# Optimization experiments

Measured on AMD Instinct MI355X. Metric: run time of the kernel, lower is better.

Reference implementation:

```python
import jax, jax.numpy as jnp
import numpy as np

B, L, D_MODEL = 2, 1024, 1024
D_STATE, D_CONV, EXPAND = 16, 4, 2
D_INNER = D_MODEL * EXPAND
LN_EPS = 1e-5


def setup_inputs() -> dict:
    key = jax.random.key(0)
    ks = jax.random.split(key, 6)
    g = lambda k, shape, scale: (jax.random.normal(k, shape, jnp.float32) * scale)
    x = jax.random.normal(ks[0], (B, L, D_MODEL), jnp.float32)
    in_proj_w = g(ks[1], (2 * D_INNER, D_MODEL), D_MODEL ** -0.5)
    conv_w = g(ks[2], (D_INNER, D_CONV), D_CONV ** -0.5)   # depthwise kernel
    conv_b = jnp.zeros((D_INNER,), jnp.float32)
    x_proj_w = g(ks[3], (2 * D_STATE + 1, D_INNER), D_INNER ** -0.5)
    A_log = jnp.tile(jnp.log(jnp.arange(1, D_STATE + 1, dtype=jnp.float32)), (D_INNER, 1))
    D_param = jnp.ones((D_INNER,), jnp.float32)
    dt_w = g(ks[4], (D_INNER, 1), 1.0)
    dt_b = jnp.full((D_INNER,), -4.0, jnp.float32)
    out_w = g(ks[5], (D_MODEL, D_INNER), D_INNER ** -0.5)
    ln_g = jnp.ones((D_INNER,), jnp.float32)
    ln_b = jnp.zeros((D_INNER,), jnp.float32)
    return dict(x=x, in_proj_w=in_proj_w, conv_w=conv_w, conv_b=conv_b,
                x_proj_w=x_proj_w, A_log=A_log, D_param=D_param,
                dt_w=dt_w, dt_b=dt_b, out_w=out_w, ln_g=ln_g, ln_b=ln_b)


def _forward(x, in_proj_w, conv_w, conv_b, x_proj_w, A_log, D_param,
             dt_w, dt_b, out_w, ln_g, ln_b):
    Lq = x.shape[1]
    xz = jnp.einsum('bld,ed->ble', x, in_proj_w)            # (B,L,2*Di)
    xb, z = xz[..., :D_INNER], xz[..., D_INNER:]
    # causal depthwise conv1d (pad left d_conv-1, valid conv == torch pad+truncate)
    xpad = jnp.pad(xb, ((0, 0), (D_CONV - 1, 0), (0, 0)))
    xc = conv_b
    for k in range(D_CONV):
        xc = xc + xpad[:, k:k + Lq, :] * conv_w[:, k]
    xb = jax.nn.silu(xc)
    proj = jnp.einsum('bld,ed->ble', xb, x_proj_w)          # (B,L,2N+1)
    dt_in = proj[..., :1]
    Bp = proj[..., 1:1 + D_STATE]                            # (B,L,N)
    Cp = proj[..., 1 + D_STATE:]                             # (B,L,N)
    dt = jax.nn.softplus(dt_in * dt_w[:, 0] + dt_b)          # (B,L,Di)
    A = -jnp.exp(A_log)                                      # (Di,N)
    dA = jnp.exp(dt[..., None] * A)                          # (B,L,Di,N)
    x_scaled = (xb * dt)[..., None] * Bp[..., None, :]       # (B,L,Di,N)
    # linear recurrence h[t] = dA[t]*h[t-1] + x_scaled[t] via associative scan
    def comb(a, b):
        return (a[0] * b[0], b[0] * a[1] + b[1])
    _, h = jax.lax.associative_scan(comb, (dA, x_scaled), axis=1)
    y = jnp.einsum('bldn,bln->bld', h, Cp) + xb * D_param    # (B,L,Di)
    mu = jnp.mean(y, axis=-1, keepdims=True)
    var = jnp.var(y, axis=-1, keepdims=True)
    y = (y - mu) / jnp.sqrt(var + LN_EPS) * ln_g + ln_b
    y = y * jax.nn.silu(z)
    return jnp.einsum('bld,ed->ble', y, out_w)               # (B,L,d_model)


def reference(x, in_proj_w, conv_w, conv_b, x_proj_w, A_log, D_param,
              dt_w, dt_b, out_w, ln_g, ln_b):
    return _forward(x, in_proj_w, conv_w, conv_b, x_proj_w, A_log, D_param,
                    dt_w, dt_b, out_w, ln_g, ln_b)
```

## Files before the change

kernel.cpp:

```cpp
#include <hip/hip_runtime.h>

typedef unsigned short u16;
typedef unsigned int u32;
typedef __bf16 bf16x8 __attribute__((ext_vector_type(8)));
typedef float f32x4 __attribute__((ext_vector_type(4)));
typedef unsigned short ushort8 __attribute__((ext_vector_type(8)));

__device__ __forceinline__ float bf2f(u16 b) {
    return __uint_as_float(((u32)b) << 16);
}
__device__ __forceinline__ u16 f2bf(float f) {
    u32 u = __float_as_uint(f);
    return (u16)((u + 0x7fffu + ((u >> 16) & 1u)) >> 16);
}

#define P_CONVW 0
#define P_CONVB 8192
#define P_ALOG  10240
#define P_DPAR  43008
#define P_DTW   45056
#define P_DTB   47104
#define P_LNG   49152
#define P_LNB   51200
#define P_TOTAL 53248

#define CCH 32
#define CT  32
#define CHUNKTOT 2097152
#define PSTRIDE 128

#define CV_X   524288
#define CV_W1  1572864
#define CV_TOT 2097152

struct ParamPtrs { const void* p[8]; };

__global__ __launch_bounds__(256) void canon_all(ParamPtrs pp, float* __restrict__ cpar,
                                                 const void* __restrict__ sx,
                                                 const void* __restrict__ sw1,
                                                 const void* __restrict__ swo,
                                                 u16* __restrict__ cx,
                                                 const void* __restrict__ sxp,
                                                 u16* __restrict__ wpad,
                                                 const u16* __restrict__ dp) {
    const bool isbf = (dp[0] != 0);
    const int blk = blockIdx.x;
    const int tid = threadIdx.x;
    if (blk < 8192) {
        const int i = blk * 256 + tid;
        const void* src;
        int off;
        if (i < CV_X)       { src = sx;  off = i; }
        else if (i < CV_W1) { src = sw1; off = i - CV_X; }
        else                { src = swo; off = i - CV_W1; }
        if (isbf) {
            ((uint2*)cx)[i] = ((const uint2*)src)[off];
        } else {
            const float4 v = ((const float4*)src)[off];
            uint2 o;
            o.x = (u32)f2bf(v.x) | ((u32)f2bf(v.y) << 16);
            o.y = (u32)f2bf(v.z) | ((u32)f2bf(v.w) << 16);
            ((uint2*)cx)[i] = o;
        }
    } else if (blk < 8400) {
        const int i = (blk - 8192) * 256 + tid;
        int seg, off;
        if (i < P_CONVB)      { seg = 0; off = i; }
        else if (i < P_ALOG)  { seg = 1; off = i - P_CONVB; }
        else if (i < P_DPAR)  { seg = 2; off = i - P_ALOG; }
        else if (i < P_DTW)   { seg = 3; off = i - P_DPAR; }
        else if (i < P_DTB)   { seg = 4; off = i - P_DTW; }
        else if (i < P_LNG)   { seg = 5; off = i - P_DTB; }
        else if (i < P_LNB)   { seg = 6; off = i - P_LNG; }
        else                  { seg = 7; off = i - P_LNB; }
        cpar[i] = isbf ? bf2f(((const u16*)pp.p[seg])[off]) : ((const float*)pp.p[seg])[off];
    } else {
        const int i = (blk - 8400) * 256 + tid;
        const int idx = i * 4;
        const int row = idx >> 11;
        u16 o[4];
#pragma unroll
        for (int q = 0; q < 4; ++q) {
            float v = 0.f;
            if (row < 33)
                v = isbf ? bf2f(((const u16*)sxp)[idx + q]) : ((const float*)sxp)[idx + q];
            o[q] = f2bf(v);
        }
        *(uint2*)&wpad[idx] = *(uint2*)o;
    }
}

__device__ __forceinline__ bf16x8 lds_frag(const char* smem, u32 base, int row, int kk,
                                           int quad, u32 xorv) {
    const u32 addr = (base + (u32)(row * 128 + kk * 64 + quad * 16)) ^ xorv;
    return *(const bf16x8*)(smem + addr);
}

template <int MODE>
__global__ __launch_bounds__(512, 2) void gemm8(const u16* __restrict__ A,
                                                const u16* __restrict__ Bw,
                                                void* __restrict__ C,
                                                int M, int N, int Kseg,
                                                int lda, int ldb) {
    extern __shared__ char smem[];
    const int bm = blockIdx.x, bn = blockIdx.y;
    const int kbase = blockIdx.z * Kseg;
    const int tid = threadIdx.x;
    const int lane = tid & 63, wave = tid >> 6;
    const int wm = wave >> 2, wn = wave & 3;
    const int l16 = lane & 15, quad = lane >> 4;
    const int NT = Kseg >> 6;
    const u32 xorv = (u32)((l16 & 7) << 4);

    const int rIss = wave * 8 + (lane >> 3);
    const int logC = (lane & 7) ^ ((lane >> 3) & 7);
    size_t aSrc[2], bSrc[4];
#pragma unroll
    for (int j = 0; j < 2; ++j)
        aSrc[j] = (size_t)(bm * 128 + j * 64 + rIss) * lda + logC * 8 + kbase;
#pragma unroll
    for (int j = 0; j < 4; ++j)
        bSrc[j] = (size_t)(bn * 256 + j * 64 + rIss) * ldb + logC * 8 + kbase;
    const u32 ldsW = (u32)(wave * 1024);

#define SG_A(slot, j, kel) __builtin_amdgcn_global_load_lds( \
        (const u32*)(A + aSrc[j] + (kel)), (u32*)(smem + (slot) + (j) * 8192 + ldsW), 16, 0, 0)
#define SG_B(slot, j, kel) __builtin_amdgcn_global_load_lds( \
        (const u32*)(Bw + bSrc[j] + (kel)), (u32*)(smem + (slot) + (j) * 8192 + ldsW), 16, 0, 0)

    const u32 sA0 = 0, sA1 = 16384, sA2 = 32768;
    const u32 sB0 = 49152, sB1 = 81920, sB2 = 114688;

    SG_A(sA0, 0, 0); SG_A(sA0, 1, 0);
    SG_B(sB0, 0, 0); SG_B(sB0, 1, 0); SG_B(sB0, 2, 0); SG_B(sB0, 3, 0);
    SG_A(sA1, 0, 64); SG_A(sA1, 1, 64);
    SG_B(sB1, 0, 64); SG_B(sB1, 1, 64); SG_B(sB1, 2, 64); SG_B(sB1, 3, 64);
    asm volatile("s_waitcnt vmcnt(6)" ::: "memory");
    __builtin_amdgcn_s_barrier();
    __builtin_amdgcn_sched_barrier(0);

    u32 curA = sA0, nxtA = sA1, stgA = sA2;
    u32 curB = sB0, nxtB = sB1, stgB = sB2;
    int kStage = 128;

    f32x4 acc[4][4] = {};
    bf16x8 a[4][2], b[4][2];

    for (int t = 0; t < NT; ++t) {
        const bool doStage = (t + 2) < NT;
#pragma unroll
        for (int mt = 0; mt < 4; ++mt)
#pragma unroll
            for (int kk = 0; kk < 2; ++kk)
                a[mt][kk] = lds_frag(smem, curA, wm * 64 + mt * 16 + l16, kk, quad, xorv);
#pragma unroll
        for (int nt = 0; nt < 2; ++nt)
#pragma unroll
            for (int kk = 0; kk < 2; ++kk)
                b[nt][kk] = lds_frag(smem, curB, wn * 64 + nt * 16 + l16, kk, quad, xorv);
        if (doStage) { SG_A(stgA, 0, kStage); SG_A(stgA, 1, kStage); SG_B(stgB, 0, kStage); }
        __builtin_amdgcn_s_setprio(1);
#pragma unroll
        for (int mt = 0; mt < 4; ++mt)
#pragma unroll
            for (int nt = 0; nt < 2; ++nt)
#pragma unroll
                for (int kk = 0; kk < 2; ++kk)
                    acc[mt][nt] = __builtin_amdgcn_mfma_f32_16x16x32_bf16(
                        a[mt][kk], b[nt][kk], acc[mt][nt], 0, 0, 0);
        __builtin_amdgcn_s_setprio(0);
#pragma unroll
        for (int nt = 2; nt < 4; ++nt)
#pragma unroll
            for (int kk = 0; kk < 2; ++kk)
                b[nt][kk] = lds_frag(smem, curB, wn * 64 + nt * 16 + l16, kk, quad, xorv);
        if (doStage) { SG_B(stgB, 1, kStage); SG_B(stgB, 2, kStage); SG_B(stgB, 3, kStage); }
        __builtin_amdgcn_s_setprio(1);
#pragma unroll
        for (int mt = 0; mt < 4; ++mt)
#pragma unroll
            for (int nt = 2; nt < 4; ++nt)
#pragma unroll
                for (int kk = 0; kk < 2; ++kk)
                    acc[mt][nt] = __builtin_amdgcn_mfma_f32_16x16x32_bf16(
                        a[mt][kk], b[nt][kk], acc[mt][nt], 0, 0, 0);
        __builtin_amdgcn_s_setprio(0);
        if (t < NT - 1) {
            if (doStage) asm volatile("s_waitcnt vmcnt(6)" ::: "memory");
            else         asm volatile("s_waitcnt vmcnt(0)" ::: "memory");
            __builtin_amdgcn_s_barrier();
            __builtin_amdgcn_sched_barrier(0);
            u32 tA = curA; curA = nxtA; nxtA = stgA; stgA = tA;
            u32 tB = curB; curB = nxtB; nxtB = stgB; stgB = tB;
            kStage += 64;
        }
    }
#undef SG_A
#undef SG_B

    float* Cf = (float*)C + (MODE == 1 ? (size_t)blockIdx.z * M * N : (size_t)0);
#pragma unroll
    for (int mt = 0; mt < 4; ++mt) {
#pragma unroll
        for (int r = 0; r < 4; ++r) {
            const int row = bm * 128 + wm * 64 + mt * 16 + quad * 4 + r;
#pragma unroll
            for (int nt = 0; nt < 4; ++nt) {
                const int col = bn * 256 + wn * 64 + nt * 16 + l16;
                if (MODE == 0)
                    ((u16*)C)[(size_t)row * N + col] = f2bf(acc[mt][nt][r]);
                else
                    Cf[(size_t)row * N + col] = acc[mt][nt][r];
            }
        }
    }
}

template <int MODE>
__global__ __launch_bounds__(256) void gemm_bt(const u16* __restrict__ A,
                                               const u16* __restrict__ Bw,
                                               void* __restrict__ C,
                                               int M, int N, int Kseg,
                                               int lda, int ldb) {
    const int bm = blockIdx.x;
    const int bn = blockIdx.y;
    const int kbase = blockIdx.z * Kseg;
    const int tid = threadIdx.x;
    const int lane = tid & 63;
    const int wave = tid >> 6;
    const int wm = wave >> 1, wn = wave & 1;
    const int l16 = lane & 15, quad = lane >> 4;

    __shared__ __align__(16) u16 sA[128 * 32];
    __shared__ __align__(16) u16 sB[128 * 32];

    f32x4 acc[4][4] = {};

    const int rsub = lane >> 2;
    const int csub = (lane & 3) * 8;

    for (int k0 = 0; k0 < Kseg; k0 += 32) {
        const int kc = kbase + k0 + csub;
        __syncthreads();
#pragma unroll
        for (int q = 0; q < 2; ++q) {
            const int g = wave + 4 * q;
            const int row = g * 16 + rsub;
            __builtin_amdgcn_global_load_lds(
                (const u32*)&A[(size_t)(bm * 128 + row) * lda + kc],
                (u32*)&sA[g * 512], 16, 0, 0);
            __builtin_amdgcn_global_load_lds(
                (const u32*)&Bw[(size_t)(bn * 128 + row) * ldb + kc],
                (u32*)&sB[g * 512], 16, 0, 0);
        }
        __syncthreads();

        bf16x8 af[4], bg[4];
#pragma unroll
        for (int t = 0; t < 4; ++t) {
            af[t] = *(const bf16x8*)&sA[(wm * 64 + t * 16 + l16) * 32 + quad * 8];
            bg[t] = *(const bf16x8*)&sB[(wn * 64 + t * 16 + l16) * 32 + quad * 8];
        }
#pragma unroll
        for (int mt = 0; mt < 4; ++mt)
#pragma unroll
            for (int nt = 0; nt < 4; ++nt)
                acc[mt][nt] = __builtin_amdgcn_mfma_f32_16x16x32_bf16(
                    af[mt], bg[nt], acc[mt][nt], 0, 0, 0);
    }

    float* Cf = (float*)C + (MODE == 1 ? (size_t)blockIdx.z * M * N : (size_t)0);
#pragma unroll
    for (int mt = 0; mt < 4; ++mt) {
#pragma unroll
        for (int r = 0; r < 4; ++r) {
            const int row = bm * 128 + wm * 64 + mt * 16 + quad * 4 + r;
#pragma unroll
            for (int nt = 0; nt < 4; ++nt) {
                const int col = bn * 128 + wn * 64 + nt * 16 + l16;
                if (MODE == 0)
                    ((u16*)C)[(size_t)row * N + col] = f2bf(acc[mt][nt][r]);
                else
                    Cf[(size_t)row * N + col] = acc[mt][nt][r];
            }
        }
    }
}

__global__ __launch_bounds__(256) void reduce_parts(const float* __restrict__ src,
                                                    float* __restrict__ dst,
                                                    int n4, int parts) {
    const int i = blockIdx.x * 256 + threadIdx.x;
    if (i >= n4) return;
    float4 s = ((const float4*)src)[i];
    for (int p = 1; p < parts; ++p) {
        const float4 v = ((const float4*)src)[(size_t)p * n4 + i];
        s.x += v.x; s.y += v.y; s.z += v.z; s.w += v.w;
    }
    ((float4*)dst)[i] = s;
}

__global__ __launch_bounds__(256) void conv_silu(const u16* __restrict__ xz,
                                                 const float* __restrict__ par,
                                                 u16* __restrict__ xb16) {
    const int idx = blockIdx.x * 256 + threadIdx.x;
    const int d8 = idx & 255;
    const int bl = idx >> 8;
    const int l = bl & 1023;
    const int d0 = d8 * 8;

    float acc[8];
    {
        const float4 b0 = *(const float4*)&par[P_CONVB + d0];
        const float4 b1 = *(const float4*)&par[P_CONVB + d0 + 4];
        acc[0] = b0.x; acc[1] = b0.y; acc[2] = b0.z; acc[3] = b0.w;
        acc[4] = b1.x; acc[5] = b1.y; acc[6] = b1.z; acc[7] = b1.w;
    }
    float warr[8][4];
#pragma unroll
    for (int q = 0; q < 8; ++q) {
        const float4 w = *(const float4*)&par[P_CONVW + (d0 + q) * 4];
        warr[q][0] = w.x; warr[q][1] = w.y; warr[q][2] = w.z; warr[q][3] = w.w;
    }
#pragma unroll
    for (int k = 0; k < 4; ++k) {
        const int ls = l + k - 3;
        if (ls >= 0) {
            const ushort8 xv = *(const ushort8*)&xz[(size_t)(bl + k - 3) * 4096 + d0];
#pragma unroll
            for (int q = 0; q < 8; ++q)
                acc[q] = fmaf(bf2f(xv[q]), warr[q][k], acc[q]);
        }
    }
    u16 o[8];
#pragma unroll
    for (int q = 0; q < 8; ++q) {
        const float s = acc[q] / (1.f + __expf(-acc[q]));
        o[q] = f2bf(s);
    }
    *(uint4*)&xb16[(size_t)bl * 2048 + d0] = *(uint4*)o;
}

__global__ __launch_bounds__(256) void scan_p1(const u16* __restrict__ xb16,
                                               const float* __restrict__ proj,
                                               const float* __restrict__ par,
                                               float* __restrict__ PS) {
    const int tid = threadIdx.x;
    const int half = tid & 1;
    const int d = blockIdx.x * 128 + (tid >> 1);
    const int c = blockIdx.y;
    const int b = blockIdx.z;
    const int nb = half * 8;
    __shared__ float sp[CT][33];
    const size_t row0 = (size_t)b * 1024 + c * CT;
    for (int f = tid; f < CT * 33; f += 256) {
        const int i = f / 33, j = f - i * 33;
        sp[i][j] = proj[(row0 + i) * PSTRIDE + j];
    }
    float Aneg[8];
#pragma unroll
    for (int n = 0; n < 8; ++n) Aneg[n] = -__expf(par[P_ALOG + d * 16 + nb + n]);
    const float dtw = par[P_DTW + d], dtb = par[P_DTB + d];
    __syncthreads();

    float h[8] = {}, P[8];
#pragma unroll
    for (int n = 0; n < 8; ++n) P[n] = 1.f;

    float xv = bf2f(xb16[row0 * 2048 + d]);
    for (int i = 0; i < CT; ++i) {
        const float xv_next = (i + 1 < CT) ? bf2f(xb16[(row0 + i + 1) * 2048 + d]) : 0.f;
        const float darg = fmaf(sp[i][0], dtw, dtb);
        const float dt = (darg > 20.f) ? darg : __logf(1.f + __expf(darg));
        const float xdt = xv * dt;
#pragma unroll
        for (int n = 0; n < 8; ++n) {
            const float dA = __expf(dt * Aneg[n]);
            P[n] *= dA;
            h[n] = fmaf(dA, h[n], xdt * sp[i][1 + nb + n]);
        }
        xv = xv_next;
    }
    const size_t base = (((size_t)b * CCH + c) * 16) * 2048 + d;
#pragma unroll
    for (int n = 0; n < 8; ++n) {
        PS[base + (size_t)(nb + n) * 2048] = P[n];
        PS[CHUNKTOT + base + (size_t)(nb + n) * 2048] = h[n];
    }
}

__global__ __launch_bounds__(256) void scan_comb(const float* __restrict__ PS,
                                                 float* __restrict__ H) {
    const int t = blockIdx.x * 256 + threadIdx.x;
    const int d = t & 2047;
    const int n = (t >> 11) & 15;
    const int b = t >> 15;
    float h = 0.f;
#pragma unroll
    for (int c = 0; c < CCH; ++c) {
        const size_t idx = (((size_t)b * CCH + c) * 16 + n) * 2048 + d;
        H[idx] = h;
        h = fmaf(PS[idx], h, PS[CHUNKTOT + idx]);
    }
}

__global__ __launch_bounds__(256) void scan_p2(const u16* __restrict__ xb16,
                                               const float* __restrict__ proj,
                                               const float* __restrict__ par,
                                               const float* __restrict__ H,
                                               u16* __restrict__ y) {
    const int tid = threadIdx.x;
    const int half = tid & 1;
    const int d = blockIdx.x * 128 + (tid >> 1);
    const int c = blockIdx.y;
    const int b = blockIdx.z;
    const int nb = half * 8;
    __shared__ float sp[CT][33];
    const size_t row0 = (size_t)b * 1024 + c * CT;
    for (int f = tid; f < CT * 33; f += 256) {
        const int i = f / 33, j = f - i * 33;
        sp[i][j] = proj[(row0 + i) * PSTRIDE + j];
    }
    float Aneg[8], h[8];
    const size_t hbase = (((size_t)b * CCH + c) * 16) * 2048 + d;
#pragma unroll
    for (int n = 0; n < 8; ++n) {
        Aneg[n] = -__expf(par[P_ALOG + d * 16 + nb + n]);
        h[n] = H[hbase + (size_t)(nb + n) * 2048];
    }
    const float dtw = par[P_DTW + d], dtb = par[P_DTB + d];
    const float Dp = par[P_DPAR + d];
    __syncthreads();

    float xv = bf2f(xb16[row0 * 2048 + d]);
    for (int i = 0; i < CT; ++i) {
        const float xv_next = (i + 1 < CT) ? bf2f(xb16[(row0 + i + 1) * 2048 + d]) : 0.f;
        const float darg = fmaf(sp[i][0], dtw, dtb);
        const float dt = (darg > 20.f) ? darg : __logf(1.f + __expf(darg));
        const float xdt = xv * dt;
        float acc = 0.f;
#pragma unroll
        for (int n = 0; n < 8; ++n) {
            const float dA = __expf(dt * Aneg[n]);
            h[n] = fmaf(dA, h[n], xdt * sp[i][1 + nb + n]);
            acc = fmaf(h[n], sp[i][17 + nb + n], acc);
        }
        acc += __shfl_xor(acc, 1);
        if (!half)
            y[(row0 + i) * 2048 + d] = f2bf(fmaf(xv, Dp, acc));
        xv = xv_next;
    }
}

__global__ __launch_bounds__(256) void ln_silu(const u16* __restrict__ y,
                                               const u16* __restrict__ xz,
                                               const float* __restrict__ par,
                                               u16* __restrict__ yn) {
    const int row = blockIdx.x;
    const int tid = threadIdx.x;
    const int lane = tid & 63, wave = tid >> 6;
    const int d0 = tid * 8;
    const ushort8 vy = *(const ushort8*)&y[(size_t)row * 2048 + d0];
    float v[8];
    float s = 0.f, s2 = 0.f;
#pragma unroll
    for (int i = 0; i < 8; ++i) {
        v[i] = bf2f(vy[i]);
        s += v[i];
        s2 = fmaf(v[i], v[i], s2);
    }
    s += __shfl_xor(s, 1); s2 += __shfl_xor(s2, 1);
    s += __shfl_xor(s, 2); s2 += __shfl_xor(s2, 2);
    s += __shfl_xor(s, 4); s2 += __shfl_xor(s2, 4);
    s += __shfl_xor(s, 8); s2 += __shfl_xor(s2, 8);
    s += __shfl_xor(s, 16); s2 += __shfl_xor(s2, 16);
    s += __shfl_xor(s, 32); s2 += __shfl_xor(s2, 32);
    __shared__ float rs[4], rs2[4];
    if (lane == 0) { rs[wave] = s; rs2[wave] = s2; }
    __syncthreads();
    const float ts = rs[0] + rs[1] + rs[2] + rs[3];
    const float ts2 = rs2[0] + rs2[1] + rs2[2] + rs2[3];
    const float mu = ts * (1.f / 2048.f);
    const float var = ts2 * (1.f / 2048.f) - mu * mu;
    const float rstd = rsqrtf(var + 1e-5f);

    const ushort8 vz = *(const ushort8*)&xz[(size_t)row * 4096 + 2048 + d0];
    float g[8], bb[8];
    {
        const float4 g0 = *(const float4*)&par[P_LNG + d0];
        const float4 g1 = *(const float4*)&par[P_LNG + d0 + 4];
        g[0] = g0.x; g[1] = g0.y; g[2] = g0.z; g[3] = g0.w;
        g[4] = g1.x; g[5] = g1.y; g[6] = g1.z; g[7] = g1.w;
        const float4 b0 = *(const float4*)&par[P_LNB + d0];
        const float4 b1 = *(const float4*)&par[P_LNB + d0 + 4];
        bb[0] = b0.x; bb[1] = b0.y; bb[2] = b0.z; bb[3] = b0.w;
        bb[4] = b1.x; bb[5] = b1.y; bb[6] = b1.z; bb[7] = b1.w;
    }
    u16 o[8];
#pragma unroll
    for (int i = 0; i < 8; ++i) {
        float t = (v[i] - mu) * rstd * g[i] + bb[i];
        const float z = bf2f(vz[i]);
        t *= z / (1.f + __expf(-z));
        o[i] = f2bf(t);
    }
    *(uint4*)&yn[(size_t)row * 2048 + d0] = *(uint4*)o;
}

extern "C" void kernel_launch(void* const* d_in, const int* in_sizes, int n_in,
                              void* d_out, int out_size, void* d_ws, size_t ws_size,
                              hipStream_t stream) {
    const void* x         = d_in[0];
    const void* in_proj_w = d_in[1];
    const void* conv_w    = d_in[2];
    const void* conv_b    = d_in[3];
    const void* x_proj_w  = d_in[4];
    const void* A_log     = d_in[5];
    const void* D_param   = d_in[6];
    const void* dt_w      = d_in[7];
    const void* dt_b      = d_in[8];
    const void* out_w     = d_in[9];
    const void* ln_g      = d_in[10];
    const void* ln_b      = d_in[11];
    const u16* dp = (const u16*)D_param;

    float* cpar = (float*)d_ws;
    u16* cx     = (u16*)(cpar + P_TOTAL);
    u16* cw1    = cx + 2097152;
    u16* cwo    = cw1 + 4194304;
    u16* xz     = cwo + 2097152;
    u16* xb16   = xz + 8388608;
    u16* y      = xb16 + 4194304;
    u16* wpad   = y + 4194304;
    float* proj = (float*)(wpad + 262144);
    float* PS   = proj + 262144;
    float* H    = PS + 2 * CHUNKTOT;
    float* gpart = H + CHUNKTOT;
    float* xpart = gpart;
    u16* yn      = xb16;

    static bool attrSet = false;
    if (!attrSet) {
        hipFuncSetAttribute(reinterpret_cast<const void*>(&gemm8<0>),
                            hipFuncAttributeMaxDynamicSharedMemorySize, 147456);
        hipFuncSetAttribute(reinterpret_cast<const void*>(&gemm8<1>),
                            hipFuncAttributeMaxDynamicSharedMemorySize, 147456);
        attrSet = true;
    }

    ParamPtrs pp;
    pp.p[0] = conv_w; pp.p[1] = conv_b; pp.p[2] = A_log; pp.p[3] = D_param;
    pp.p[4] = dt_w;   pp.p[5] = dt_b;   pp.p[6] = ln_g;  pp.p[7] = ln_b;
    canon_all<<<8656, 256, 0, stream>>>(pp, cpar, x, in_proj_w, out_w, cx,
                                        x_proj_w, wpad, dp);

    gemm8<0><<<dim3(16, 16, 1), 512, 147456, stream>>>(cx, cw1, xz,
                                                       2048, 4096, 1024, 1024, 1024);
    conv_silu<<<2048, 256, 0, stream>>>(xz, cpar, xb16);
    gemm_bt<1><<<dim3(16, 1, 16), 256, 0, stream>>>(xb16, wpad, xpart, 2048, 128, 128, 2048, 2048);
    reduce_parts<<<256, 256, 0, stream>>>(xpart, proj, 65536, 16);
    scan_p1<<<dim3(16, CCH, 2), 256, 0, stream>>>(xb16, proj, cpar, PS);
    scan_comb<<<256, 256, 0, stream>>>(PS, H);
    scan_p2<<<dim3(16, CCH, 2), 256, 0, stream>>>(xb16, proj, cpar, H, y);
    ln_silu<<<2048, 256, 0, stream>>>(y, xz, cpar, yn);
    gemm8<1><<<dim3(16, 4, 4), 512, 147456, stream>>>(yn, cwo, gpart,
                                                      2048, 1024, 512, 2048, 2048);
    reduce_parts<<<2048, 256, 0, stream>>>(gpart, (float*)d_out, 524288, 4);
}
```

Measured before the change: 234.3 us.

## Fuse chunked scan passes into one kernel with in-block chunk combine

Replaces the three-kernel chunked scan (partial pass, global combine, second pass) with a single kernel. Each block handles 4 channels across all chunks, combines the chunk carries in shared memory, and reads proj directly from global memory instead of staging it in LDS. This removes the PS/H global round trips and two launches, at the cost of fewer, differently shaped blocks and uncoalesced strided xb16 reads. It also halves the split-K factor of the output GEMM, giving fewer partial sums to reduce.

```diff
diff --git a/kernel.cpp b/kernel.cpp
--- a/kernel.cpp
+++ b/kernel.cpp
@@ -341,114 +341,106 @@
     *(uint4*)&xb16[(size_t)bl * 2048 + d0] = *(uint4*)o;
 }
 
-__global__ __launch_bounds__(256) void scan_p1(const u16* __restrict__ xb16,
-                                               const float* __restrict__ proj,
-                                               const float* __restrict__ par,
-                                               float* __restrict__ PS) {
+__global__ __launch_bounds__(256) void scan_fused(const u16* __restrict__ xb16,
+                                                  const float* __restrict__ proj,
+                                                  const float* __restrict__ par,
+                                                  u16* __restrict__ y) {
     const int tid = threadIdx.x;
-    const int half = tid & 1;
-    const int d = blockIdx.x * 128 + (tid >> 1);
-    const int c = blockIdx.y;
+    const int h2 = tid & 1;
+    const int dsub = (tid >> 1) & 3;
+    const int c = tid >> 3;
+    const int d = blockIdx.x * 4 + dsub;
     const int b = blockIdx.z;
-    const int nb = half * 8;
-    __shared__ float sp[CT][33];
-    const size_t row0 = (size_t)b * 1024 + c * CT;
-    for (int f = tid; f < CT * 33; f += 256) {
-        const int i = f / 33, j = f - i * 33;
-        sp[i][j] = proj[(row0 + i) * PSTRIDE + j];
-    }
+    const int nb = h2 * 8;
+
+    __shared__ float Pl[CCH][4][17];
+    __shared__ float Sl[CCH][4][17];
+
     float Aneg[8];
 #pragma unroll
     for (int n = 0; n < 8; ++n) Aneg[n] = -__expf(par[P_ALOG + d * 16 + nb + n]);
     const float dtw = par[P_DTW + d], dtb = par[P_DTB + d];
+    const float Dp = par[P_DPAR + d];
+
+    const size_t row0 = (size_t)b * 1024 + (size_t)c * CT;
+
+    {
+        float hl[8] = {}, P[8];
+#pragma unroll
+        for (int n = 0; n < 8; ++n) P[n] = 1.f;
+        float xv = bf2f(xb16[row0 * 2048 + d]);
+        for (int i = 0; i < CT; ++i) {
+            const float xv_next = (i + 1 < CT) ? bf2f(xb16[(row0 + i + 1) * 2048 + d]) : 0.f;
+            const size_t pb = (row0 + i) * PSTRIDE;
+            const float dtin = proj[pb];
+            const float4 q0 = *(const float4*)&proj[pb + nb + 0];
+            const float4 q1 = *(const float4*)&proj[pb + nb + 4];
+            const float4 q2 = *(const float4*)&proj[pb + nb + 8];
+            const float Bv[8] = {q0.y, q0.z, q0.w, q1.x, q1.y, q1.z, q1.w, q2.x};
+            const float darg = fmaf(dtin, dtw, dtb);
+            const float dt = (darg > 20.f) ? darg : __logf(1.f + __expf(darg));
+            const float xdt = xv * dt;
+#pragma unroll
+            for (int n = 0; n < 8; ++n) {
+                const float dA = __expf(dt * Aneg[n]);
+                P[n] *= dA;
+                hl[n] = fmaf(dA, hl[n], xdt * Bv[n]);
+            }
+            xv = xv_next;
+        }
+#pragma unroll
+        for (int n = 0; n < 8; ++n) {
+            Pl[c][dsub][nb + n] = P[n];
+            Sl[c][dsub][nb + n] = hl[n];
+        }
+    }
     __syncthreads();
 
-    float h[8] = {}, P[8];
-#pragma unroll
-    for (int n = 0; n < 8; ++n) P[n] = 1.f;
-
-    float xv = bf2f(xb16[row0 * 2048 + d]);
-    for (int i = 0; i < CT; ++i) {
-        const float xv_next = (i + 1 < CT) ? bf2f(xb16[(row0 + i + 1) * 2048 + d]) : 0.f;
-        const float darg = fmaf(sp[i][0], dtw, dtb);
-        const float dt = (darg > 20.f) ? darg : __logf(1.f + __expf(darg));
-        const float xdt = xv * dt;
-#pragma unroll
-        for (int n = 0; n < 8; ++n) {
-            const float dA = __expf(dt * Aneg[n]);
-            P[n] *= dA;
-            h[n] = fmaf(dA, h[n], xdt * sp[i][1 + nb + n]);
-        }
-        xv = xv_next;
-    }
-    const size_t base = (((size_t)b * CCH + c) * 16) * 2048 + d;
-#pragma unroll
-    for (int n = 0; n < 8; ++n) {
-        PS[base + (size_t)(nb + n) * 2048] = P[n];
-        PS[CHUNKTOT + base + (size_t)(nb + n) * 2048] = h[n];
-    }
-}
-
-__global__ __launch_bounds__(256) void scan_comb(const float* __restrict__ PS,
-                                                 float* __restrict__ H) {
-    const int t = blockIdx.x * 256 + threadIdx.x;
-    const int d = t & 2047;
-    const int n = (t >> 11) & 15;
-    const int b = t >> 15;
-    float h = 0.f;
-#pragma unroll
-    for (int c = 0; c < CCH; ++c) {
-        const size_t idx = (((size_t)b * CCH + c) * 16 + n) * 2048 + d;
-        H[idx] = h;
-        h = fmaf(PS[idx], h, PS[CHUNKTOT + idx]);
-    }
-}
-
-__global__ __launch_bounds__(256) void scan_p2(const u16* __restrict__ xb16,
-                                               const float* __restrict__ proj,
-                                               const float* __restrict__ par,
-                                               const float* __restrict__ H,
-                                               u16* __restrict__ y) {
-    const int tid = threadIdx.x;
-    const int half = tid & 1;
-    const int d = blockIdx.x * 128 + (tid >> 1);
-    const int c = blockIdx.y;
-    const int b = blockIdx.z;
-    const int nb = half * 8;
-    __shared__ float sp[CT][33];
-    const size_t row0 = (size_t)b * 1024 + c * CT;
-    for (int f = tid; f < CT * 33; f += 256) {
-        const int i = f / 33, j = f - i * 33;
-        sp[i][j] = proj[(row0 + i) * PSTRIDE + j];
-    }
-    float Aneg[8], h[8];
-    const size_t hbase = (((size_t)b * CCH + c) * 16) * 2048 + d;
-#pragma unroll
-    for (int n = 0; n < 8; ++n) {
-        Aneg[n] = -__expf(par[P_ALOG + d * 16 + nb + n]);
-        h[n] = H[hbase + (size_t)(nb + n) * 2048];
-    }
-    const float dtw = par[P_DTW + d], dtb = par[P_DTB + d];
-    const float Dp = par[P_DPAR + d];
+    if (tid < 64) {
+        const int dd = tid >> 4, n = tid & 15;
+        float hh = 0.f;
+#pragma unroll
+        for (int cc = 0; cc < CCH; ++cc) {
+            const float p = Pl[cc][dd][n];
+            const float s = Sl[cc][dd][n];
+            Pl[cc][dd][n] = hh;
+            hh = fmaf(p, hh, s);
+        }
+    }
     __syncthreads();
 
-    float xv = bf2f(xb16[row0 * 2048 + d]);
-    for (int i = 0; i < CT; ++i) {
-        const float xv_next = (i + 1 < CT) ? bf2f(xb16[(row0 + i + 1) * 2048 + d]) : 0.f;
-        const float darg = fmaf(sp[i][0], dtw, dtb);
-        const float dt = (darg > 20.f) ? darg : __logf(1.f + __expf(darg));
-        const float xdt = xv * dt;
-        float acc = 0.f;
-#pragma unroll
-        for (int n = 0; n < 8; ++n) {
-            const float dA = __expf(dt * Aneg[n]);
-            h[n] = fmaf(dA, h[n], xdt * sp[i][1 + nb + n]);
-            acc = fmaf(h[n], sp[i][17 + nb + n], acc);
-        }
-        acc += __shfl_xor(acc, 1);
-        if (!half)
-            y[(row0 + i) * 2048 + d] = f2bf(fmaf(xv, Dp, acc));
-        xv = xv_next;
+    {
+        float hl[8];
+#pragma unroll
+        for (int n = 0; n < 8; ++n) hl[n] = Pl[c][dsub][nb + n];
+        float xv = bf2f(xb16[row0 * 2048 + d]);
+        for (int i = 0; i < CT; ++i) {
+            const float xv_next = (i + 1 < CT) ? bf2f(xb16[(row0 + i + 1) * 2048 + d]) : 0.f;
+            const size_t pb = (row0 + i) * PSTRIDE;
+            const float dtin = proj[pb];
+            const float4 q0 = *(const float4*)&proj[pb + nb + 0];
+            const float4 q1 = *(const float4*)&proj[pb + nb + 4];
+            const float4 q2 = *(const float4*)&proj[pb + nb + 8];
+            const float4 r0 = *(const float4*)&proj[pb + 16 + nb + 0];
+            const float4 r1 = *(const float4*)&proj[pb + 16 + nb + 4];
+            const float4 r2 = *(const float4*)&proj[pb + 16 + nb + 8];
+            const float Bv[8] = {q0.y, q0.z, q0.w, q1.x, q1.y, q1.z, q1.w, q2.x};
+            const float Cv[8] = {r0.y, r0.z, r0.w, r1.x, r1.y, r1.z, r1.w, r2.x};
+            const float darg = fmaf(dtin, dtw, dtb);
+            const float dt = (darg > 20.f) ? darg : __logf(1.f + __expf(darg));
+            const float xdt = xv * dt;
+            float acc = 0.f;
+#pragma unroll
+            for (int n = 0; n < 8; ++n) {
+                const float dA = __expf(dt * Aneg[n]);
+                hl[n] = fmaf(dA, hl[n], xdt * Bv[n]);
+                acc = fmaf(hl[n], Cv[n], acc);
+            }
+            acc += __shfl_xor(acc, 1);
+            if (!h2)
+                y[(row0 + i) * 2048 + d] = f2bf(fmaf(xv, Dp, acc));
+            xv = xv_next;
+        }
     }
 }
 
@@ -559,11 +551,9 @@
     conv_silu<<<2048, 256, 0, stream>>>(xz, cpar, xb16);
     gemm_bt<1><<<dim3(16, 1, 16), 256, 0, stream>>>(xb16, wpad, xpart, 2048, 128, 128, 2048, 2048);
     reduce_parts<<<256, 256, 0, stream>>>(xpart, proj, 65536, 16);
-    scan_p1<<<dim3(16, CCH, 2), 256, 0, stream>>>(xb16, proj, cpar, PS);
-    scan_comb<<<256, 256, 0, stream>>>(PS, H);
-    scan_p2<<<dim3(16, CCH, 2), 256, 0, stream>>>(xb16, proj, cpar, H, y);
+    scan_fused<<<dim3(512, 1, 2), 256, 0, stream>>>(xb16, proj, cpar, y);
     ln_silu<<<2048, 256, 0, stream>>>(y, xz, cpar, yn);
-    gemm8<1><<<dim3(16, 4, 4), 512, 147456, stream>>>(yn, cwo, gpart,
-                                                      2048, 1024, 512, 2048, 2048);
-    reduce_parts<<<2048, 256, 0, stream>>>(gpart, (float*)d_out, 524288, 4);
-}
+    gemm8<1><<<dim3(16, 4, 2), 512, 147456, stream>>>(yn, cwo, gpart,
+                                                      2048, 1024, 1024, 2048, 2048);
+    reduce_parts<<<2048, 256, 0, stream>>>(gpart, (float*)d_out, 524288, 2);
+}
```

Result: no change. 233.3 us (-0.4%).
